# Performance work log

Hardware: AMD Instinct MI355X
Metric: run time of the kernel (lower is better)

The kernel has to match this reference:

```python
import jax, jax.numpy as jnp
import numpy as np

N, E, B = 50000, 800000, 512
IN, H, OUT = 128, 64, 32
BN_EPS = 1e-5


def setup_inputs() -> dict:
    key = jax.random.key(0)
    ks = jax.random.split(key, 32)
    inp = {}
    inp["x"] = jax.random.normal(ks[0], (N, IN), dtype=jnp.float32)
    inp["edge_index"] = jax.random.randint(ks[1], (2, E), 0, N, dtype=jnp.int64)
    inp["batch"] = jnp.sort(jax.random.randint(ks[2], (N,), 0, B, dtype=jnp.int64))
    inp["batch_size"] = B
    # GINConv MLP params: Linear(cin,H) -> BN(H) -> ReLU -> Linear(H,H)
    cins = [IN, H, H]
    ki = 3
    for i, cin in enumerate(cins):
        inp[f"c{i}_W1"] = jax.random.normal(ks[ki], (cin, H), dtype=jnp.float32) / np.sqrt(cin); ki += 1
        inp[f"c{i}_b1"] = jnp.zeros((H,), jnp.float32)
        inp[f"c{i}_g1"] = jnp.ones((H,), jnp.float32)
        inp[f"c{i}_bt1"] = jnp.zeros((H,), jnp.float32)
        inp[f"c{i}_W2"] = jax.random.normal(ks[ki], (H, H), dtype=jnp.float32) / np.sqrt(H); ki += 1
        inp[f"c{i}_b2"] = jnp.zeros((H,), jnp.float32)
    # final MLP (norm=None): Linear(H,H) -> ReLU -> [dropout, eval: identity] -> Linear(H,OUT)
    inp["f_W1"] = jax.random.normal(ks[ki], (H, H), dtype=jnp.float32) / np.sqrt(H); ki += 1
    inp["f_b1"] = jnp.zeros((H,), jnp.float32)
    inp["f_W2"] = jax.random.normal(ks[ki], (H, OUT), dtype=jnp.float32) / np.sqrt(H)
    inp["f_b2"] = jnp.zeros((OUT,), jnp.float32)
    return inp


def _bn(h, g, bt):
    # BatchNorm1d, training-mode statistics (biased variance), eps=1e-5
    mean = h.mean(axis=0)
    var = ((h - mean) ** 2).mean(axis=0)
    return g * (h - mean) * jax.lax.rsqrt(var + BN_EPS) + bt


def _gin_conv(x, src, dst, W1, b1, g1, bt1, W2, b2):
    # sum-aggregate neighbor features: agg[i] = sum_{(j->i)} x[j]
    agg = jax.ops.segment_sum(x[src], dst, num_segments=N)  # [N,H_in]
    h = x + agg  # (1+eps)*x + agg, eps=0
    h = jax.nn.relu(_bn(h @ W1 + b1, g1, bt1))
    return h @ W2 + b2


def reference(x, edge_index, batch, batch_size,
              c0_W1, c0_b1, c0_g1, c0_bt1, c0_W2, c0_b2,
              c1_W1, c1_b1, c1_g1, c1_bt1, c1_W2, c1_b2,
              c2_W1, c2_b1, c2_g1, c2_bt1, c2_W2, c2_b2,
              f_W1, f_b1, f_W2, f_b2):
    src, dst = edge_index[0], edge_index[1]
    convs = [(c0_W1, c0_b1, c0_g1, c0_bt1, c0_W2, c0_b2),
             (c1_W1, c1_b1, c1_g1, c1_bt1, c1_W2, c1_b2),
             (c2_W1, c2_b1, c2_g1, c2_bt1, c2_W2, c2_b2)]
    for p in convs:
        x = jax.nn.relu(_gin_conv(x, src, dst, *p))
    # global_add_pool over graph ids
    pooled = jax.ops.segment_sum(x, batch, num_segments=batch_size)  # [B,H]
    h = jax.nn.relu(pooled @ f_W1 + f_b1)  # dropout=0.5 skipped (eval mode)
    return h @ f_W2 + f_b2  # [B,OUT]
```

## Files before the change

### kernel.cpp

```cpp
#include <hip/hip_runtime.h>
#include <hip/hip_fp16.h>

#define NN 50000
#define EE 800000
#define BB 512
#define DIN 128
#define HH 64
#define DOUT 32
#define BN_EPS 1e-5f
#define SCAN_BLOCKS 196
#define GATHER_BLOCKS 1024

template <int CIN>
__global__ __launch_bounds__(256) void proj_kernel(const float* __restrict__ X,
                                                   const float* __restrict__ W,
                                                   __half2* __restrict__ Qh)
{
    __shared__ float sW[CIN * 64];
    __shared__ float sX[16 * CIN];
    const int tid = threadIdx.x;
    const int row0 = blockIdx.x * 16;

    for (int i = tid; i < CIN * 16; i += 256)
        ((float4*)sW)[i] = ((const float4*)W)[i];
    const float* Xb = X + (size_t)row0 * CIN;
    for (int i = tid; i < 16 * CIN / 4; i += 256)
        ((float4*)sX)[i] = ((const float4*)Xb)[i];
    __syncthreads();

    const int col2 = tid & 31;
    const int rg   = tid >> 5;
    float2 acc0 = {0.f, 0.f};
    float2 acc1 = {0.f, 0.f};
    const float* x0p = &sX[(rg * 2 + 0) * CIN];
    const float* x1p = &sX[(rg * 2 + 1) * CIN];
#pragma unroll 4
    for (int k = 0; k < CIN; ++k) {
        const float2 w = *(const float2*)&sW[k * 64 + col2 * 2];
        const float x0 = x0p[k];
        const float x1 = x1p[k];
        acc0.x = fmaf(x0, w.x, acc0.x);
        acc0.y = fmaf(x0, w.y, acc0.y);
        acc1.x = fmaf(x1, w.x, acc1.x);
        acc1.y = fmaf(x1, w.y, acc1.y);
    }
    const int r0 = row0 + rg * 2;
    Qh[(size_t)(r0 + 0) * 32 + col2] = __floats2half2_rn(acc0.x, acc0.y);
    Qh[(size_t)(r0 + 1) * 32 + col2] = __floats2half2_rn(acc1.x, acc1.y);
}

__global__ __launch_bounds__(256) void hist_rank_kernel(const int* __restrict__ dst,
                                                        int* __restrict__ deg,
                                                        unsigned short* __restrict__ rank)
{
    const int e = blockIdx.x * 256 + threadIdx.x;
    rank[e] = (unsigned short)atomicAdd(&deg[dst[e]], 1);
}

__global__ __launch_bounds__(256) void scanA_kernel(const int* __restrict__ deg,
                                                    int* __restrict__ offs,
                                                    int* __restrict__ blockSums)
{
    __shared__ int s[256];
    const int t = threadIdx.x;
    const int i = blockIdx.x * 256 + t;
    const int v = (i < NN) ? deg[i] : 0;
    s[t] = v;
    __syncthreads();
    for (int off = 1; off < 256; off <<= 1) {
        const int a = (t >= off) ? s[t - off] : 0;
        __syncthreads();
        s[t] += a;
        __syncthreads();
    }
    if (i < NN) offs[i] = s[t] - v;
    if (t == 255) blockSums[blockIdx.x] = s[255];
}

__global__ __launch_bounds__(256) void scanB_kernel(const int* __restrict__ blockSums,
                                                    int* __restrict__ blockOff)
{
    __shared__ int s[256];
    const int t = threadIdx.x;
    const int v = (t < SCAN_BLOCKS) ? blockSums[t] : 0;
    s[t] = v;
    __syncthreads();
    for (int off = 1; off < 256; off <<= 1) {
        const int a = (t >= off) ? s[t - off] : 0;
        __syncthreads();
        s[t] += a;
        __syncthreads();
    }
    if (t < SCAN_BLOCKS) blockOff[t] = s[t] - v;
}

__global__ __launch_bounds__(256) void scanC_kernel(int* __restrict__ offs,
                                                    const int* __restrict__ blockOff,
                                                    float* __restrict__ statsbuf,
                                                    float* __restrict__ pooled)
{
    const int i = blockIdx.x * 256 + threadIdx.x;
    if (i < NN) offs[i] += blockOff[blockIdx.x];
    if (i == 0) offs[NN] = EE;
    if (i < 384) statsbuf[i] = 0.f;
    if (i < BB * 64) pooled[i] = 0.f;
}

__global__ __launch_bounds__(256) void scatter_kernel(const int* __restrict__ src,
                                                      const int* __restrict__ dst,
                                                      const unsigned short* __restrict__ rank,
                                                      const int* __restrict__ offs,
                                                      unsigned short* __restrict__ srcSorted)
{
    const int e = blockIdx.x * 256 + threadIdx.x;
    const int pos = offs[dst[e]] + (int)rank[e];
    srcSorted[pos] = (unsigned short)src[e];
}

__global__ __launch_bounds__(256) void gather_kernel(const __half2* __restrict__ Qh,
                                                     const int* __restrict__ offs,
                                                     const unsigned short* __restrict__ srcSorted,
                                                     const float* __restrict__ b1,
                                                     float* __restrict__ Z,
                                                     float* __restrict__ sums,
                                                     float* __restrict__ sumsq)
{
    const int tid  = threadIdx.x;
    const int lane = tid & 63;
    const int wid  = tid >> 6;
    const int colq = lane & 15;
    const int grp  = lane >> 4;
    const uint2* Qr = (const uint2*)Qh;
    const float4 bb = ((const float4*)b1)[colq];

    float sa0 = 0.f, sa1 = 0.f, sa2 = 0.f, sa3 = 0.f;
    float ta0 = 0.f, ta1 = 0.f, ta2 = 0.f, ta3 = 0.f;

    for (int node = blockIdx.x * 4 + wid; node < NN; node += GATHER_BLOCKS * 4) {
        const int o0 = offs[node];
        const int o1 = offs[node + 1];
        float a0 = 0.f, a1 = 0.f, a2 = 0.f, a3 = 0.f;
        int j = o0;
        for (; j + 16 <= o1; j += 16) {
            const int e0 = srcSorted[j + grp];
            const int e1 = srcSorted[j + 4 + grp];
            const int e2 = srcSorted[j + 8 + grp];
            const int e3 = srcSorted[j + 12 + grp];
            const uint2 r0 = Qr[(size_t)e0 * 16 + colq];
            const uint2 r1 = Qr[(size_t)e1 * 16 + colq];
            const uint2 r2 = Qr[(size_t)e2 * 16 + colq];
            const uint2 r3 = Qr[(size_t)e3 * 16 + colq];
            float2 p;
            p = __half22float2(*(const __half2*)&r0.x); a0 += p.x; a1 += p.y;
            p = __half22float2(*(const __half2*)&r0.y); a2 += p.x; a3 += p.y;
            p = __half22float2(*(const __half2*)&r1.x); a0 += p.x; a1 += p.y;
            p = __half22float2(*(const __half2*)&r1.y); a2 += p.x; a3 += p.y;
            p = __half22float2(*(const __half2*)&r2.x); a0 += p.x; a1 += p.y;
            p = __half22float2(*(const __half2*)&r2.y); a2 += p.x; a3 += p.y;
            p = __half22float2(*(const __half2*)&r3.x); a0 += p.x; a1 += p.y;
            p = __half22float2(*(const __half2*)&r3.y); a2 += p.x; a3 += p.y;
        }
        for (; j + 4 <= o1; j += 4) {
            const int e0 = srcSorted[j + grp];
            const uint2 r0 = Qr[(size_t)e0 * 16 + colq];
            float2 p;
            p = __half22float2(*(const __half2*)&r0.x); a0 += p.x; a1 += p.y;
            p = __half22float2(*(const __half2*)&r0.y); a2 += p.x; a3 += p.y;
        }
        if (grp < o1 - j) {
            const int e0 = srcSorted[j + grp];
            const uint2 r0 = Qr[(size_t)e0 * 16 + colq];
            float2 p;
            p = __half22float2(*(const __half2*)&r0.x); a0 += p.x; a1 += p.y;
            p = __half22float2(*(const __half2*)&r0.y); a2 += p.x; a3 += p.y;
        }
        a0 += __shfl_xor(a0, 16); a1 += __shfl_xor(a1, 16);
        a2 += __shfl_xor(a2, 16); a3 += __shfl_xor(a3, 16);
        a0 += __shfl_xor(a0, 32); a1 += __shfl_xor(a1, 32);
        a2 += __shfl_xor(a2, 32); a3 += __shfl_xor(a3, 32);
        if (grp == 0) {
            const uint2 sr = Qr[(size_t)node * 16 + colq];
            float2 p;
            p = __half22float2(*(const __half2*)&sr.x); a0 += p.x + bb.x; a1 += p.y + bb.y;
            p = __half22float2(*(const __half2*)&sr.y); a2 += p.x + bb.z; a3 += p.y + bb.w;
            float4 zv = {a0, a1, a2, a3};
            ((float4*)Z)[(size_t)node * 16 + colq] = zv;
            sa0 += a0; sa1 += a1; sa2 += a2; sa3 += a3;
            ta0 += a0 * a0; ta1 += a1 * a1; ta2 += a2 * a2; ta3 += a3 * a3;
        }
    }

    __shared__ float red[4][16][8];
    if (grp == 0) {
        float* rp = red[wid][colq];
        rp[0] = sa0; rp[1] = sa1; rp[2] = sa2; rp[3] = sa3;
        rp[4] = ta0; rp[5] = ta1; rp[6] = ta2; rp[7] = ta3;
    }
    __syncthreads();
    if (tid < 128) {
        const int cq = tid >> 3;
        const int k  = tid & 7;
        const float v = red[0][cq][k] + red[1][cq][k] + red[2][cq][k] + red[3][cq][k];
        float* dstp = (k < 4) ? &sums[cq * 4 + k] : &sumsq[cq * 4 + (k - 4)];
        atomicAdd(dstp, v);
    }
}

template <bool POOL>
__global__ __launch_bounds__(256) void gemm2_kernel(const float* __restrict__ Z,
                                                    const float* __restrict__ sums,
                                                    const float* __restrict__ sumsq,
                                                    const float* __restrict__ g1,
                                                    const float* __restrict__ bt1,
                                                    const float* __restrict__ W2,
                                                    const float* __restrict__ b2,
                                                    const int* __restrict__ batch,
                                                    float* __restrict__ out)
{
    __shared__ float sW[64 * 64];
    __shared__ float sH[16 * 64];
    __shared__ float sScale[64];
    __shared__ float sShift[64];
    const int tid = threadIdx.x;
    const int row0 = blockIdx.x * 16;

    if (tid < 64) {
        const float inv_n = 1.0f / (float)NN;
        const float mean = sums[tid] * inv_n;
        const float var = fmaxf(sumsq[tid] * inv_n - mean * mean, 0.f);
        const float sc = g1[tid] * rsqrtf(var + BN_EPS);
        sScale[tid] = sc;
        sShift[tid] = bt1[tid] - mean * sc;
    }
    for (int i = tid; i < 64 * 16; i += 256)
        ((float4*)sW)[i] = ((const float4*)W2)[i];
    __syncthreads();

    const float4* Zb = (const float4*)(Z + (size_t)row0 * 64);
    {
        const int i = tid;
        const float4 z = Zb[i];
        const int c4 = i & 15;
        const float4 sc = ((const float4*)sScale)[c4];
        const float4 sh = ((const float4*)sShift)[c4];
        float4 h;
        h.x = fmaxf(fmaf(z.x, sc.x, sh.x), 0.f);
        h.y = fmaxf(fmaf(z.y, sc.y, sh.y), 0.f);
        h.z = fmaxf(fmaf(z.z, sc.z, sh.z), 0.f);
        h.w = fmaxf(fmaf(z.w, sc.w, sh.w), 0.f);
        ((float4*)sH)[i] = h;
    }
    __syncthreads();

    const int col = tid & 63;
    const int r0  = tid >> 6;
    const float bc = b2[col];
    float acc[4] = {bc, bc, bc, bc};
    for (int k = 0; k < 64; k += 4) {
        const float w0 = sW[(k + 0) * 64 + col];
        const float w1 = sW[(k + 1) * 64 + col];
        const float w2 = sW[(k + 2) * 64 + col];
        const float w3 = sW[(k + 3) * 64 + col];
#pragma unroll
        for (int rr = 0; rr < 4; ++rr) {
            const float4 hv = *(const float4*)&sH[(r0 + rr * 4) * 64 + k];
            acc[rr] = fmaf(hv.x, w0, acc[rr]);
            acc[rr] = fmaf(hv.y, w1, acc[rr]);
            acc[rr] = fmaf(hv.z, w2, acc[rr]);
            acc[rr] = fmaf(hv.w, w3, acc[rr]);
        }
    }
#pragma unroll
    for (int rr = 0; rr < 4; ++rr) {
        const int row = row0 + r0 + rr * 4;
        const float v = fmaxf(acc[rr], 0.f);
        if (POOL) {
            atomicAdd(&out[(size_t)batch[row] * 64 + col], v);
        } else {
            out[(size_t)row * 64 + col] = v;
        }
    }
}

__global__ __launch_bounds__(256) void final_mlp(const float* __restrict__ P,
                                                 const float* __restrict__ W1,
                                                 const float* __restrict__ b1,
                                                 const float* __restrict__ W2,
                                                 const float* __restrict__ b2,
                                                 float* __restrict__ out)
{
    __shared__ float sW1[64 * 64];
    __shared__ float sW2[64 * 32];
    __shared__ float sH[4 * 64];
    const int tid = threadIdx.x;
    const int row0 = blockIdx.x * 4;

    for (int i = tid; i < 1024; i += 256) ((float4*)sW1)[i] = ((const float4*)W1)[i];
    for (int i = tid; i < 512; i += 256) ((float4*)sW2)[i] = ((const float4*)W2)[i];
    __syncthreads();

    const int col = tid & 63;
    const int r = tid >> 6;
    float acc = b1[col];
    const float* prow = P + (size_t)(row0 + r) * 64;
    for (int k = 0; k < 64; ++k) acc = fmaf(prow[k], sW1[k * 64 + col], acc);
    sH[r * 64 + col] = fmaxf(acc, 0.f);
    __syncthreads();

    if (tid < 128) {
        const int c = tid & 31;
        const int r2 = tid >> 5;
        float a2 = b2[c];
        for (int k = 0; k < 64; ++k) a2 = fmaf(sH[r2 * 64 + k], sW2[k * 32 + c], a2);
        out[(size_t)(row0 + r2) * 32 + c] = a2;
    }
}

extern "C" void kernel_launch(void* const* d_in, const int* in_sizes, int n_in,
                              void* d_out, int out_size, void* d_ws, size_t ws_size,
                              hipStream_t stream)
{
    const float* x   = (const float*)d_in[0];
    const int* ei    = (const int*)d_in[1];
    const int* batch = (const int*)d_in[2];
    const float* cW1[3] = {(const float*)d_in[4],  (const float*)d_in[10], (const float*)d_in[16]};
    const float* cb1[3] = {(const float*)d_in[5],  (const float*)d_in[11], (const float*)d_in[17]};
    const float* cg1[3] = {(const float*)d_in[6],  (const float*)d_in[12], (const float*)d_in[18]};
    const float* cbt[3] = {(const float*)d_in[7],  (const float*)d_in[13], (const float*)d_in[19]};
    const float* cW2[3] = {(const float*)d_in[8],  (const float*)d_in[14], (const float*)d_in[20]};
    const float* cb2[3] = {(const float*)d_in[9],  (const float*)d_in[15], (const float*)d_in[21]};
    const float* fW1 = (const float*)d_in[22];
    const float* fb1 = (const float*)d_in[23];
    const float* fW2 = (const float*)d_in[24];
    const float* fb2 = (const float*)d_in[25];
    float* out = (float*)d_out;

    float* bufX     = (float*)d_ws;
    __half2* Qh     = (__half2*)(bufX + (size_t)NN * 64);
    float* pooled   = (float*)(Qh + (size_t)NN * 32);
    float* statsbuf = pooled + (size_t)BB * 64;
    int* deg        = (int*)(statsbuf + 384);
    int* offs       = deg + NN;
    int* blockSums  = offs + (NN + 1);
    int* blockOff   = blockSums + 256;
    unsigned short* rank      = (unsigned short*)(blockOff + 256);
    unsigned short* srcSorted = rank + EE;

    const int* esrc = ei;
    const int* edst = ei + EE;

    const int gemm_blocks = NN / 16;
    const int edge_blocks = EE / 256;

    hipMemsetAsync(deg, 0, NN * sizeof(int), stream);
    hist_rank_kernel<<<edge_blocks, 256, 0, stream>>>(edst, deg, rank);
    scanA_kernel<<<SCAN_BLOCKS, 256, 0, stream>>>(deg, offs, blockSums);
    scanB_kernel<<<1, 256, 0, stream>>>(blockSums, blockOff);
    scanC_kernel<<<SCAN_BLOCKS, 256, 0, stream>>>(offs, blockOff, statsbuf, pooled);
    scatter_kernel<<<edge_blocks, 256, 0, stream>>>(esrc, edst, rank, offs, srcSorted);

    for (int layer = 0; layer < 3; ++layer) {
        float* sums  = statsbuf + layer * 128;
        float* sumsq = sums + 64;

        if (layer == 0)
            proj_kernel<DIN><<<gemm_blocks, 256, 0, stream>>>(x, cW1[0], Qh);
        else
            proj_kernel<HH><<<gemm_blocks, 256, 0, stream>>>(bufX, cW1[layer], Qh);

        gather_kernel<<<GATHER_BLOCKS, 256, 0, stream>>>(Qh, offs, srcSorted, cb1[layer],
                                                         bufX, sums, sumsq);

        if (layer < 2) {
            gemm2_kernel<false><<<gemm_blocks, 256, 0, stream>>>(bufX, sums, sumsq, cg1[layer],
                                                                 cbt[layer], cW2[layer], cb2[layer],
                                                                 nullptr, bufX);
        } else {
            gemm2_kernel<true><<<gemm_blocks, 256, 0, stream>>>(bufX, sums, sumsq, cg1[layer],
                                                                cbt[layer], cW2[layer], cb2[layer],
                                                                batch, pooled);
        }
    }

    final_mlp<<<BB / 4, 256, 0, stream>>>(pooled, fW1, fb1, fW2, fb2, out);
}
```

Before: 341.8 us.

## Batch 12 gathers per lane with zero-row padding for tail edges

The gather loop now loads 12 neighbor indices and 12 fp16 feature rows per lane before accumulating, which raises memory-level parallelism. Tail edges are handled branch-free by pointing them at an extra zeroed row appended to the projected buffer. The gather grid is also doubled to 2048 blocks. The cost is more registers per thread and wasted loads on the zero row for low-degree nodes (average degree is 16, so many nodes take only the padded pass).

```diff
diff --git a/kernel.cpp b/kernel.cpp
--- a/kernel.cpp
+++ b/kernel.cpp
@@ -9,7 +9,7 @@
 #define DOUT 32
 #define BN_EPS 1e-5f
 #define SCAN_BLOCKS 196
-#define GATHER_BLOCKS 1024
+#define GATHER_BLOCKS 2048
 
 template <int CIN>
 __global__ __launch_bounds__(256) void proj_kernel(const float* __restrict__ X,
@@ -97,13 +97,15 @@
 __global__ __launch_bounds__(256) void scanC_kernel(int* __restrict__ offs,
                                                     const int* __restrict__ blockOff,
                                                     float* __restrict__ statsbuf,
-                                                    float* __restrict__ pooled)
+                                                    float* __restrict__ pooled,
+                                                    unsigned int* __restrict__ qzero)
 {
     const int i = blockIdx.x * 256 + threadIdx.x;
     if (i < NN) offs[i] += blockOff[blockIdx.x];
     if (i == 0) offs[NN] = EE;
     if (i < 384) statsbuf[i] = 0.f;
     if (i < BB * 64) pooled[i] = 0.f;
+    if (blockIdx.x == 1 && threadIdx.x < 32) qzero[threadIdx.x] = 0u;
 }
 
 __global__ __launch_bounds__(256) void scatter_kernel(const int* __restrict__ src,
@@ -141,38 +143,38 @@
         const int o1 = offs[node + 1];
         float a0 = 0.f, a1 = 0.f, a2 = 0.f, a3 = 0.f;
         int j = o0;
-        for (; j + 16 <= o1; j += 16) {
-            const int e0 = srcSorted[j + grp];
-            const int e1 = srcSorted[j + 4 + grp];
-            const int e2 = srcSorted[j + 8 + grp];
-            const int e3 = srcSorted[j + 12 + grp];
-            const uint2 r0 = Qr[(size_t)e0 * 16 + colq];
-            const uint2 r1 = Qr[(size_t)e1 * 16 + colq];
-            const uint2 r2 = Qr[(size_t)e2 * 16 + colq];
-            const uint2 r3 = Qr[(size_t)e3 * 16 + colq];
-            float2 p;
-            p = __half22float2(*(const __half2*)&r0.x); a0 += p.x; a1 += p.y;
-            p = __half22float2(*(const __half2*)&r0.y); a2 += p.x; a3 += p.y;
-            p = __half22float2(*(const __half2*)&r1.x); a0 += p.x; a1 += p.y;
-            p = __half22float2(*(const __half2*)&r1.y); a2 += p.x; a3 += p.y;
-            p = __half22float2(*(const __half2*)&r2.x); a0 += p.x; a1 += p.y;
-            p = __half22float2(*(const __half2*)&r2.y); a2 += p.x; a3 += p.y;
-            p = __half22float2(*(const __half2*)&r3.x); a0 += p.x; a1 += p.y;
-            p = __half22float2(*(const __half2*)&r3.y); a2 += p.x; a3 += p.y;
-        }
-        for (; j + 4 <= o1; j += 4) {
-            const int e0 = srcSorted[j + grp];
-            const uint2 r0 = Qr[(size_t)e0 * 16 + colq];
-            float2 p;
-            p = __half22float2(*(const __half2*)&r0.x); a0 += p.x; a1 += p.y;
-            p = __half22float2(*(const __half2*)&r0.y); a2 += p.x; a3 += p.y;
-        }
-        if (grp < o1 - j) {
-            const int e0 = srcSorted[j + grp];
-            const uint2 r0 = Qr[(size_t)e0 * 16 + colq];
-            float2 p;
-            p = __half22float2(*(const __half2*)&r0.x); a0 += p.x; a1 += p.y;
-            p = __half22float2(*(const __half2*)&r0.y); a2 += p.x; a3 += p.y;
+        while (o1 - j > 48) {
+            int idx[12];
+#pragma unroll
+            for (int k = 0; k < 12; ++k) idx[k] = srcSorted[j + k * 4 + grp];
+            uint2 r[12];
+#pragma unroll
+            for (int k = 0; k < 12; ++k) r[k] = Qr[(size_t)idx[k] * 16 + colq];
+#pragma unroll
+            for (int k = 0; k < 12; ++k) {
+                float2 p;
+                p = __half22float2(*(const __half2*)&r[k].x); a0 += p.x; a1 += p.y;
+                p = __half22float2(*(const __half2*)&r[k].y); a2 += p.x; a3 += p.y;
+            }
+            j += 48;
+        }
+        {
+            int idx[12];
+#pragma unroll
+            for (int k = 0; k < 12; ++k) {
+                const int p = j + k * 4 + grp;
+                const int v = srcSorted[p];
+                idx[k] = (p < o1) ? v : NN;
+            }
+            uint2 r[12];
+#pragma unroll
+            for (int k = 0; k < 12; ++k) r[k] = Qr[(size_t)idx[k] * 16 + colq];
+#pragma unroll
+            for (int k = 0; k < 12; ++k) {
+                float2 p;
+                p = __half22float2(*(const __half2*)&r[k].x); a0 += p.x; a1 += p.y;
+                p = __half22float2(*(const __half2*)&r[k].y); a2 += p.x; a3 += p.y;
+            }
         }
         a0 += __shfl_xor(a0, 16); a1 += __shfl_xor(a1, 16);
         a2 += __shfl_xor(a2, 16); a3 += __shfl_xor(a3, 16);
@@ -337,7 +339,7 @@
 
     float* bufX     = (float*)d_ws;
     __half2* Qh     = (__half2*)(bufX + (size_t)NN * 64);
-    float* pooled   = (float*)(Qh + (size_t)NN * 32);
+    float* pooled   = (float*)(Qh + (size_t)(NN + 1) * 32);
     float* statsbuf = pooled + (size_t)BB * 64;
     int* deg        = (int*)(statsbuf + 384);
     int* offs       = deg + NN;
@@ -356,7 +358,8 @@
     hist_rank_kernel<<<edge_blocks, 256, 0, stream>>>(edst, deg, rank);
     scanA_kernel<<<SCAN_BLOCKS, 256, 0, stream>>>(deg, offs, blockSums);
     scanB_kernel<<<1, 256, 0, stream>>>(blockSums, blockOff);
-    scanC_kernel<<<SCAN_BLOCKS, 256, 0, stream>>>(offs, blockOff, statsbuf, pooled);
+    scanC_kernel<<<SCAN_BLOCKS, 256, 0, stream>>>(offs, blockOff, statsbuf, pooled,
+                                                  (unsigned int*)(Qh + (size_t)NN * 32));
     scatter_kernel<<<edge_blocks, 256, 0, stream>>>(esrc, edst, rank, offs, srcSorted);
 
     for (int layer = 0; layer < 3; ++layer) {
```

After: 382.4 us. +11.9%, slower.

## Fuse next-layer projection into gemm2 and region-partition the CSR scatter

Applied to the files above, without the earlier changes.

For the first two layers, the second MLP linear (BN+ReLU, W2, ReLU) is fused with the next layer's W1 projection, writing half-precision Qh directly. This removes the fp32 bufX round trip and the separate proj kernel launch. The scatter kernel now assigns each block an edge chunk and a destination region, so writes to srcSorted land in a localized range. The cost is that every edge's dst is read 8 times. Nontemporal loads and stores are added in the histogram kernel.

```diff
diff --git a/kernel.cpp b/kernel.cpp
--- a/kernel.cpp
+++ b/kernel.cpp
@@ -10,6 +10,8 @@
 #define BN_EPS 1e-5f
 #define SCAN_BLOCKS 196
 #define GATHER_BLOCKS 1024
+#define REGSZ 6250
+#define ECHUNK 3125
 
 template <int CIN>
 __global__ __launch_bounds__(256) void proj_kernel(const float* __restrict__ X,
@@ -54,7 +56,9 @@
                                                         unsigned short* __restrict__ rank)
 {
     const int e = blockIdx.x * 256 + threadIdx.x;
-    rank[e] = (unsigned short)atomicAdd(&deg[dst[e]], 1);
+    const int d = __builtin_nontemporal_load(dst + e);
+    const unsigned short r = (unsigned short)atomicAdd(&deg[d], 1);
+    __builtin_nontemporal_store(r, rank + e);
 }
 
 __global__ __launch_bounds__(256) void scanA_kernel(const int* __restrict__ deg,
@@ -112,9 +116,18 @@
                                                       const int* __restrict__ offs,
                                                       unsigned short* __restrict__ srcSorted)
 {
-    const int e = blockIdx.x * 256 + threadIdx.x;
-    const int pos = offs[dst[e]] + (int)rank[e];
-    srcSorted[pos] = (unsigned short)src[e];
+    const int region = blockIdx.x & 7;
+    const int chunk  = blockIdx.x >> 3;
+    const int base   = chunk * ECHUNK;
+    const int lo = region * REGSZ;
+    for (int e = base + threadIdx.x; e < base + ECHUNK; e += 256) {
+        const int d = __builtin_nontemporal_load(dst + e);
+        if ((unsigned)(d - lo) < REGSZ) {
+            const int s = src[e];
+            const int r = (int)rank[e];
+            srcSorted[offs[d] + r] = (unsigned short)s;
+        }
+    }
 }
 
 __global__ __launch_bounds__(256) void gather_kernel(const __half2* __restrict__ Qh,
@@ -206,19 +219,20 @@
     }
 }
 
-template <bool POOL>
-__global__ __launch_bounds__(256) void gemm2_kernel(const float* __restrict__ Z,
-                                                    const float* __restrict__ sums,
-                                                    const float* __restrict__ sumsq,
-                                                    const float* __restrict__ g1,
-                                                    const float* __restrict__ bt1,
-                                                    const float* __restrict__ W2,
-                                                    const float* __restrict__ b2,
-                                                    const int* __restrict__ batch,
-                                                    float* __restrict__ out)
-{
-    __shared__ float sW[64 * 64];
+__global__ __launch_bounds__(256) void gemm2proj_kernel(const float* __restrict__ Z,
+                                                        const float* __restrict__ sums,
+                                                        const float* __restrict__ sumsq,
+                                                        const float* __restrict__ g1,
+                                                        const float* __restrict__ bt1,
+                                                        const float* __restrict__ W2,
+                                                        const float* __restrict__ b2,
+                                                        const float* __restrict__ W1n,
+                                                        __half2* __restrict__ QhOut)
+{
+    __shared__ float sW2[64 * 64];
+    __shared__ float sW1[64 * 64];
     __shared__ float sH[16 * 64];
+    __shared__ float sA[16 * 64];
     __shared__ float sScale[64];
     __shared__ float sShift[64];
     const int tid = threadIdx.x;
@@ -232,7 +246,102 @@
         sScale[tid] = sc;
         sShift[tid] = bt1[tid] - mean * sc;
     }
-    for (int i = tid; i < 64 * 16; i += 256)
+    for (int i = tid; i < 1024; i += 256) {
+        ((float4*)sW2)[i] = ((const float4*)W2)[i];
+        ((float4*)sW1)[i] = ((const float4*)W1n)[i];
+    }
+    __syncthreads();
+
+    const float4* Zb = (const float4*)(Z + (size_t)row0 * 64);
+    {
+        const int i = tid;
+        const float4 z = Zb[i];
+        const int c4 = i & 15;
+        const float4 sc = ((const float4*)sScale)[c4];
+        const float4 sh = ((const float4*)sShift)[c4];
+        float4 h;
+        h.x = fmaxf(fmaf(z.x, sc.x, sh.x), 0.f);
+        h.y = fmaxf(fmaf(z.y, sc.y, sh.y), 0.f);
+        h.z = fmaxf(fmaf(z.z, sc.z, sh.z), 0.f);
+        h.w = fmaxf(fmaf(z.w, sc.w, sh.w), 0.f);
+        ((float4*)sH)[i] = h;
+    }
+    __syncthreads();
+
+    {
+        const int col = tid & 63;
+        const int r0  = tid >> 6;
+        const float bc = b2[col];
+        float acc[4] = {bc, bc, bc, bc};
+        for (int k = 0; k < 64; k += 4) {
+            const float w0 = sW2[(k + 0) * 64 + col];
+            const float w1 = sW2[(k + 1) * 64 + col];
+            const float w2 = sW2[(k + 2) * 64 + col];
+            const float w3 = sW2[(k + 3) * 64 + col];
+#pragma unroll
+            for (int rr = 0; rr < 4; ++rr) {
+                const float4 hv = *(const float4*)&sH[(r0 + rr * 4) * 64 + k];
+                acc[rr] = fmaf(hv.x, w0, acc[rr]);
+                acc[rr] = fmaf(hv.y, w1, acc[rr]);
+                acc[rr] = fmaf(hv.z, w2, acc[rr]);
+                acc[rr] = fmaf(hv.w, w3, acc[rr]);
+            }
+        }
+#pragma unroll
+        for (int rr = 0; rr < 4; ++rr)
+            sA[(r0 + rr * 4) * 64 + col] = fmaxf(acc[rr], 0.f);
+    }
+    __syncthreads();
+
+    {
+        const int col2 = tid & 31;
+        const int rg   = tid >> 5;
+        float2 acc0 = {0.f, 0.f};
+        float2 acc1 = {0.f, 0.f};
+        const float* a0p = &sA[(rg * 2 + 0) * 64];
+        const float* a1p = &sA[(rg * 2 + 1) * 64];
+#pragma unroll 4
+        for (int k = 0; k < 64; ++k) {
+            const float2 w = *(const float2*)&sW1[k * 64 + col2 * 2];
+            const float a0 = a0p[k];
+            const float a1 = a1p[k];
+            acc0.x = fmaf(a0, w.x, acc0.x);
+            acc0.y = fmaf(a0, w.y, acc0.y);
+            acc1.x = fmaf(a1, w.x, acc1.x);
+            acc1.y = fmaf(a1, w.y, acc1.y);
+        }
+        const int r0 = row0 + rg * 2;
+        QhOut[(size_t)(r0 + 0) * 32 + col2] = __floats2half2_rn(acc0.x, acc0.y);
+        QhOut[(size_t)(r0 + 1) * 32 + col2] = __floats2half2_rn(acc1.x, acc1.y);
+    }
+}
+
+__global__ __launch_bounds__(256) void gemm2pool_kernel(const float* __restrict__ Z,
+                                                        const float* __restrict__ sums,
+                                                        const float* __restrict__ sumsq,
+                                                        const float* __restrict__ g1,
+                                                        const float* __restrict__ bt1,
+                                                        const float* __restrict__ W2,
+                                                        const float* __restrict__ b2,
+                                                        const int* __restrict__ batch,
+                                                        float* __restrict__ out)
+{
+    __shared__ float sW[64 * 64];
+    __shared__ float sH[16 * 64];
+    __shared__ float sScale[64];
+    __shared__ float sShift[64];
+    const int tid = threadIdx.x;
+    const int row0 = blockIdx.x * 16;
+
+    if (tid < 64) {
+        const float inv_n = 1.0f / (float)NN;
+        const float mean = sums[tid] * inv_n;
+        const float var = fmaxf(sumsq[tid] * inv_n - mean * mean, 0.f);
+        const float sc = g1[tid] * rsqrtf(var + BN_EPS);
+        sScale[tid] = sc;
+        sShift[tid] = bt1[tid] - mean * sc;
+    }
+    for (int i = tid; i < 1024; i += 256)
         ((float4*)sW)[i] = ((const float4*)W2)[i];
     __syncthreads();
 
@@ -274,11 +383,7 @@
     for (int rr = 0; rr < 4; ++rr) {
         const int row = row0 + r0 + rr * 4;
         const float v = fmaxf(acc[rr], 0.f);
-        if (POOL) {
-            atomicAdd(&out[(size_t)batch[row] * 64 + col], v);
-        } else {
-            out[(size_t)row * 64 + col] = v;
-        }
+        atomicAdd(&out[(size_t)batch[row] * 64 + col], v);
     }
 }
 
@@ -357,28 +462,25 @@
     scanA_kernel<<<SCAN_BLOCKS, 256, 0, stream>>>(deg, offs, blockSums);
     scanB_kernel<<<1, 256, 0, stream>>>(blockSums, blockOff);
     scanC_kernel<<<SCAN_BLOCKS, 256, 0, stream>>>(offs, blockOff, statsbuf, pooled);
-    scatter_kernel<<<edge_blocks, 256, 0, stream>>>(esrc, edst, rank, offs, srcSorted);
+    scatter_kernel<<<2048, 256, 0, stream>>>(esrc, edst, rank, offs, srcSorted);
+
+    proj_kernel<DIN><<<gemm_blocks, 256, 0, stream>>>(x, cW1[0], Qh);
 
     for (int layer = 0; layer < 3; ++layer) {
         float* sums  = statsbuf + layer * 128;
         float* sumsq = sums + 64;
 
-        if (layer == 0)
-            proj_kernel<DIN><<<gemm_blocks, 256, 0, stream>>>(x, cW1[0], Qh);
-        else
-            proj_kernel<HH><<<gemm_blocks, 256, 0, stream>>>(bufX, cW1[layer], Qh);
-
         gather_kernel<<<GATHER_BLOCKS, 256, 0, stream>>>(Qh, offs, srcSorted, cb1[layer],
                                                          bufX, sums, sumsq);
 
         if (layer < 2) {
-            gemm2_kernel<false><<<gemm_blocks, 256, 0, stream>>>(bufX, sums, sumsq, cg1[layer],
-                                                                 cbt[layer], cW2[layer], cb2[layer],
-                                                                 nullptr, bufX);
+            gemm2proj_kernel<<<gemm_blocks, 256, 0, stream>>>(bufX, sums, sumsq, cg1[layer],
+                                                              cbt[layer], cW2[layer], cb2[layer],
+                                                              cW1[layer + 1], Qh);
         } else {
-            gemm2_kernel<true><<<gemm_blocks, 256, 0, stream>>>(bufX, sums, sumsq, cg1[layer],
-                                                                cbt[layer], cW2[layer], cb2[layer],
-                                                                batch, pooled);
+            gemm2pool_kernel<<<gemm_blocks, 256, 0, stream>>>(bufX, sums, sumsq, cg1[layer],
+                                                              cbt[layer], cW2[layer], cb2[layer],
+                                                              batch, pooled);
         }
     }
 
```

Measured after the change: 348.2 us. About the same (+1.9%).
